# Performance work log

Hardware: AMD Instinct MI355X
Metric: run time of the kernel (lower is better)

Reference implementation:

```python
import jax, jax.numpy as jnp
from jax import lax
import numpy as np

V, E, H = 32000, 128, 256
B, S = 256, 256
A, SA = 8, 32


def gru_last(tokens, lengths, emb, Wih, Whh, bih, bhh):
    """PyTorch-GRU over padded [B,S] tokens; returns hidden at step lengths-1 ([B,H])."""
    Bb, Ss = tokens.shape
    Hh = Whh.shape[1]
    x = emb[tokens]                                   # [B,S,E]
    gi = jnp.einsum('bse,ge->bsg', x, Wih) + bih      # input gates precomputed [B,S,3H]
    lengths = jnp.maximum(lengths, 1)
    mask = jnp.arange(Ss)[None, :] < lengths[:, None]  # [B,S] valid-step mask

    def step(h, inp):
        gi_t, m_t = inp                               # [B,3H], [B]
        gh = h @ Whh.T + bhh                          # [B,3H]
        ir, iz, inn = jnp.split(gi_t, 3, axis=-1)
        hr, hz, hn = jnp.split(gh, 3, axis=-1)
        r = jax.nn.sigmoid(ir + hr)
        z = jax.nn.sigmoid(iz + hz)
        n = jnp.tanh(inn + r * hn)
        h_new = (1.0 - z) * n + z * h
        h = jnp.where(m_t[:, None], h_new, h)          # freeze past length (packed-seq semantics)
        return h, None

    h0 = jnp.zeros((Bb, Hh), x.dtype)
    hT, _ = lax.scan(step, h0, (gi.transpose(1, 0, 2), mask.T))
    return hT


def setup_inputs() -> dict:
    key = jax.random.key(0)
    ks = jax.random.split(key, 16)
    sc = 0.05
    inp = {
        'obs_tokens':  jax.random.randint(ks[0], (B, S), 0, V),
        'obs_len':     jax.random.randint(ks[1], (B,), 1, S + 1),
        'look_tokens': jax.random.randint(ks[2], (B, S), 0, V),
        'look_len':    jax.random.randint(ks[3], (B,), 1, S + 1),
        'inv_tokens':  jax.random.randint(ks[4], (B, S), 0, V),
        'inv_len':     jax.random.randint(ks[5], (B,), 1, S + 1),
        'act_tokens':  jax.random.randint(ks[6], (B * A, SA), 0, V),
        'act_len':     jax.random.randint(ks[7], (B * A,), 1, SA + 1),
        'emb':  jax.random.normal(ks[8], (V, E), jnp.float32) * sc,
        # stacked GRU params for [obs, look, inv, act] encoders
        'Wih':  jax.random.normal(ks[9],  (4, 3 * H, E), jnp.float32) * sc,
        'Whh':  jax.random.normal(ks[10], (4, 3 * H, H), jnp.float32) * sc,
        'bih':  jax.random.normal(ks[11], (4, 3 * H), jnp.float32) * sc,
        'bhh':  jax.random.normal(ks[12], (4, 3 * H), jnp.float32) * sc,
        'hidden_W': jax.random.normal(ks[13], (H, 4 * H), jnp.float32) * sc,
        'hidden_b': jnp.zeros((H,), jnp.float32),
        'scorer_W': jax.random.normal(ks[14], (1, H), jnp.float32) * sc,
        'scorer_b': jnp.zeros((1,), jnp.float32),
    }
    return inp


def reference(obs_tokens, obs_len, look_tokens, look_len, inv_tokens, inv_len,
              act_tokens, act_len, emb, Wih, Whh, bih, bhh,
              hidden_W, hidden_b, scorer_W, scorer_b):
    obs_out  = gru_last(obs_tokens,  obs_len,  emb, Wih[0], Whh[0], bih[0], bhh[0])
    look_out = gru_last(look_tokens, look_len, emb, Wih[1], Whh[1], bih[1], bhh[1])
    inv_out  = gru_last(inv_tokens,  inv_len,  emb, Wih[2], Whh[2], bih[2], bhh[2])
    act_out  = gru_last(act_tokens,  act_len,  emb, Wih[3], Whh[3], bih[3], bhh[3])

    state = jnp.concatenate([obs_out, look_out, inv_out], axis=1)  # [B,3H]
    n_act = act_tokens.shape[0] // obs_tokens.shape[0]
    state_rep = jnp.repeat(state, n_act, axis=0)                    # [B*A,3H]
    z = jax.nn.relu(jnp.concatenate([state_rep, act_out], axis=1) @ hidden_W.T + hidden_b)
    q = (z @ scorer_W.T + scorer_b)[:, 0]                           # [B*A]
    return q.reshape(obs_tokens.shape[0], n_act)                    # per-state q-values [B,A]
```

## Files before the change

### kernel.cpp

```cpp
#include <hip/hip_runtime.h>
#include <math.h>

#define VSZ 32000
#define EDIM 128
#define HDIM 256
#define BSZ 256
#define SLEN 256
#define ANUM 8
#define SALEN 32
#define G3 768
#define TB 16
#define PADW 392

#define WB_SHORTS (4 * 12 * 8 * 6 * 2 * 512)
#define KK_STRIDE (8 * 6 * 2 * 512)
#define WV_STRIDE (6 * 2 * 512)
#define OFF_HWT   (WB_SHORTS / 2)
#define HWT_SIZE  (1024 * HDIM)
#define OFF_STATE (OFF_HWT + HWT_SIZE)
#define OFF_ACT   (OFF_STATE + BSZ * G3)

typedef __attribute__((ext_vector_type(8))) short bf16x8;
typedef __attribute__((ext_vector_type(4))) short bf16x4;
typedef __attribute__((ext_vector_type(4))) float f32x4;

__device__ __forceinline__ unsigned short bf16_rne(float f) {
    unsigned int u = __builtin_bit_cast(unsigned int, f);
    unsigned int r = (u + 0x7FFFu + ((u >> 16) & 1u)) >> 16;
    return (unsigned short)r;
}
__device__ __forceinline__ float bf16_to_f32(unsigned short h) {
    unsigned int u = ((unsigned int)h) << 16;
    return __builtin_bit_cast(float, u);
}

__global__ void prep_frag(const float* __restrict__ Wih, const float* __restrict__ Whh,
                          unsigned short* __restrict__ WB) {
    int idx = blockIdx.x * 256 + threadIdx.x;
    int q = idx & 7;
    int l = (idx >> 3) & 63;
    int rest = idx >> 9;
    int slot = rest % 6; rest /= 6;
    int wv = rest & 7;   rest >>= 3;
    int kk = rest % 12;
    int enc = rest / 12;
    int cc2 = slot / 3, g3 = slot % 3;
    int row = 256 * g3 + 16 * (wv + 8 * cc2) + (l & 15);
    int kloc = 8 * (l >> 4) + q;
    float v;
    if (kk < 4) v = Wih[(enc * G3 + row) * EDIM + 32 * kk + kloc];
    else        v = Whh[(enc * G3 + row) * HDIM + 32 * (kk - 4) + kloc];
    unsigned short hi = bf16_rne(v);
    unsigned short lo = bf16_rne(v - bf16_to_f32(hi));
    size_t base = ((((size_t)(enc * 12 + kk) * 8 + wv) * 6 + slot) * 2) * 512 + l * 8 + q;
    WB[base] = hi;
    WB[base + 512] = lo;
}

__global__ void prep_hwt(const float* __restrict__ hW, float* __restrict__ hWT) {
    int idx = blockIdx.x * 256 + threadIdx.x;
    if (idx >= HWT_SIZE) return;
    int k = idx >> 8;
    int j = idx & 255;
    hWT[idx] = hW[j * 1024 + k];
}

__global__ void __launch_bounds__(1024, 1)
gru_mfma(const int* __restrict__ obs_t, const int* __restrict__ obs_l,
         const int* __restrict__ look_t, const int* __restrict__ look_l,
         const int* __restrict__ inv_t, const int* __restrict__ inv_l,
         const int* __restrict__ act_t, const int* __restrict__ act_l,
         const float* __restrict__ emb, const float* __restrict__ bih,
         const float* __restrict__ bhh, const unsigned short* __restrict__ WB,
         float* __restrict__ state, float* __restrict__ act_out) {
    const int bid = blockIdx.x;
    const int x = bid & 7, rr = bid >> 3;
    int enc, tile, S;
    const int* toks;
    const int* lens;
    if (x < 6 && rr < 8) {
        enc = x >> 1; tile = (x & 1) * 8 + rr; S = SLEN;
        toks = (enc == 0) ? obs_t : (enc == 1) ? look_t : inv_t;
        lens = (enc == 0) ? obs_l : (enc == 1) ? look_l : inv_l;
    } else {
        enc = 3; S = SALEN;
        tile = (x >= 6) ? (rr * 2 + (x - 6)) : (44 + (rr - 8) * 6 + x);
        toks = act_t; lens = act_l;
    }
    const int tid = threadIdx.x;
    const int l   = tid & 63;
    const int w   = tid >> 6;
    const int wvb = w & 7;
    const int c2  = w >> 3;
    const int lr  = l & 15;
    const int lg  = l >> 4;
    const int j   = 16 * wvb + 128 * c2 + lr;

    __shared__ __align__(16) unsigned short xh_hi[TB][PADW];
    __shared__ __align__(16) unsigned short xh_lo[TB][PADW];

    if (tid < 512) {
        int m = tid >> 5, c = tid & 31;
#pragma unroll
        for (int q = 0; q < 8; ++q) {
            xh_hi[m][EDIM + 8 * c + q] = 0;
            xh_lo[m][EDIM + 8 * c + q] = 0;
        }
    }

    int maxlen = 1;
    for (int s = 0; s < TB; ++s) {
        int L = lens[tile * TB + s];
        if (L < 1) L = 1;
        if (L > maxlen) maxlen = L;
    }
    int lenm[4];
#pragma unroll
    for (int i = 0; i < 4; ++i) {
        int L = lens[tile * TB + 4 * lg + i];
        lenm[i] = (L < 1) ? 1 : L;
    }

    const float bR  = bih[enc * G3 + j] + bhh[enc * G3 + j];
    const float bZ  = bih[enc * G3 + 256 + j] + bhh[enc * G3 + 256 + j];
    const float bIN = bih[enc * G3 + 512 + j];
    const float bHN = bhh[enc * G3 + 512 + j];

    float hO[4];
#pragma unroll
    for (int i = 0; i < 4; ++i) hO[i] = 0.f;

    auto stage = [&](int tt) {
        if (tid < 512) {
            int m = tid >> 5, g = tid & 31;
            int tok = toks[(tile * TB + m) * S + tt];
            const float4 v = *(const float4*)(emb + (size_t)tok * EDIM + g * 4);
            float vv[4] = {v.x, v.y, v.z, v.w};
            bf16x4 H, Lo;
#pragma unroll
            for (int q = 0; q < 4; ++q) {
                unsigned short h16 = bf16_rne(vv[q]);
                H[q]  = (short)h16;
                Lo[q] = (short)bf16_rne(vv[q] - bf16_to_f32(h16));
            }
            *(bf16x4*)(&xh_hi[m][g * 4]) = H;
            *(bf16x4*)(&xh_lo[m][g * 4]) = Lo;
        }
    };

    const unsigned short* WBw = WB + (size_t)enc * (12 * KK_STRIDE)
                                   + wvb * WV_STRIDE + (c2 * 3) * 1024 + l * 8;

    stage(0);
    __syncthreads();

    for (int t = 0; t < maxlen; ++t) {
        f32x4 aR  = (f32x4){bR, bR, bR, bR};
        f32x4 aZ  = (f32x4){bZ, bZ, bZ, bZ};
        f32x4 aNX = (f32x4){bIN, bIN, bIN, bIN};
        f32x4 aNH = (f32x4){bHN, bHN, bHN, bHN};

#pragma unroll 2
        for (int kk = 0; kk < 12; ++kk) {
            const int off = (kk < 4) ? 32 * kk : EDIM + 32 * (kk - 4);
            bf16x8 Ahi = *(const bf16x8*)(&xh_hi[lr][off + 8 * lg]);
            bf16x8 Alo = *(const bf16x8*)(&xh_lo[lr][off + 8 * lg]);
            const unsigned short* wb = WBw + (size_t)kk * KK_STRIDE;
            bf16x8 BhR = *(const bf16x8*)(wb);
            bf16x8 BhZ = *(const bf16x8*)(wb + 1024);
            bf16x8 BhN = *(const bf16x8*)(wb + 2048);
            aR = __builtin_amdgcn_mfma_f32_16x16x32_bf16(Ahi, BhR, aR, 0, 0, 0);
            aR = __builtin_amdgcn_mfma_f32_16x16x32_bf16(Alo, BhR, aR, 0, 0, 0);
            aZ = __builtin_amdgcn_mfma_f32_16x16x32_bf16(Ahi, BhZ, aZ, 0, 0, 0);
            aZ = __builtin_amdgcn_mfma_f32_16x16x32_bf16(Alo, BhZ, aZ, 0, 0, 0);
            if (kk < 4) {
                aNX = __builtin_amdgcn_mfma_f32_16x16x32_bf16(Ahi, BhN, aNX, 0, 0, 0);
                aNX = __builtin_amdgcn_mfma_f32_16x16x32_bf16(Alo, BhN, aNX, 0, 0, 0);
            } else {
                aNH = __builtin_amdgcn_mfma_f32_16x16x32_bf16(Ahi, BhN, aNH, 0, 0, 0);
                aNH = __builtin_amdgcn_mfma_f32_16x16x32_bf16(Alo, BhN, aNH, 0, 0, 0);
            }
        }

        __syncthreads();

#pragma unroll
        for (int i = 0; i < 4; ++i) {
            int m = 4 * lg + i;
            float r = 1.f / (1.f + expf(-aR[i]));
            float z = 1.f / (1.f + expf(-aZ[i]));
            float n = tanhf(aNX[i] + r * aNH[i]);
            float hv = (1.f - z) * n + z * hO[i];
            hv = (t < lenm[i]) ? hv : hO[i];
            hO[i] = hv;
            unsigned short h16 = bf16_rne(hv);
            xh_hi[m][EDIM + j] = h16;
            xh_lo[m][EDIM + j] = bf16_rne(hv - bf16_to_f32(h16));
        }
        if (t + 1 < maxlen) stage(t + 1);
        __syncthreads();
    }

#pragma unroll
    for (int i = 0; i < 4; ++i) {
        int sg = tile * TB + 4 * lg + i;
        if (enc < 3) state[sg * G3 + enc * HDIM + j] = hO[i];
        else         act_out[sg * HDIM + j] = hO[i];
    }
}

__global__ void __launch_bounds__(256)
mlp_kernel(const float* __restrict__ state, const float* __restrict__ act_out,
           const float* __restrict__ hWT, const float* __restrict__ hb,
           const float* __restrict__ sW, const float* __restrict__ sb,
           float* __restrict__ q) {
    int b = blockIdx.x;
    int j = threadIdx.x;
    __shared__ float st[G3];
    __shared__ float ab[ANUM][HDIM];
#pragma unroll
    for (int i = 0; i < 3; ++i) st[i * 256 + j] = state[b * G3 + i * 256 + j];
#pragma unroll
    for (int i = 0; i < ANUM; ++i) ab[i][j] = act_out[(b * ANUM + i) * HDIM + j];
    __syncthreads();

    float accS = 0.f;
#pragma unroll 4
    for (int k = 0; k < G3; ++k) accS += st[k] * hWT[k * HDIM + j];

    float accA[ANUM];
#pragma unroll
    for (int i = 0; i < ANUM; ++i) accA[i] = 0.f;
    for (int k = 0; k < HDIM; ++k) {
        float w = hWT[(G3 + k) * HDIM + j];
#pragma unroll
        for (int i = 0; i < ANUM; ++i) accA[i] += ab[i][k] * w;
    }

    float base = hb[j] + accS;
    float p[ANUM];
#pragma unroll
    for (int i = 0; i < ANUM; ++i) {
        float zz = base + accA[i];
        zz = zz > 0.f ? zz : 0.f;
        p[i] = zz * sW[j];
    }

    __shared__ float wsum[ANUM][4];
#pragma unroll
    for (int i = 0; i < ANUM; ++i) {
        float v = p[i];
        for (int off = 32; off >= 1; off >>= 1) v += __shfl_down(v, off, 64);
        if ((j & 63) == 0) wsum[i][j >> 6] = v;
    }
    __syncthreads();
    if (j < ANUM) q[b * ANUM + j] = wsum[j][0] + wsum[j][1] + wsum[j][2] + wsum[j][3] + sb[0];
}

extern "C" void kernel_launch(void* const* d_in, const int* in_sizes, int n_in,
                              void* d_out, int out_size, void* d_ws, size_t ws_size,
                              hipStream_t stream) {
    const int* obs_t  = (const int*)d_in[0];
    const int* obs_l  = (const int*)d_in[1];
    const int* look_t = (const int*)d_in[2];
    const int* look_l = (const int*)d_in[3];
    const int* inv_t  = (const int*)d_in[4];
    const int* inv_l  = (const int*)d_in[5];
    const int* act_t  = (const int*)d_in[6];
    const int* act_l  = (const int*)d_in[7];
    const float* emb  = (const float*)d_in[8];
    const float* Wih  = (const float*)d_in[9];
    const float* Whh  = (const float*)d_in[10];
    const float* bih  = (const float*)d_in[11];
    const float* bhh  = (const float*)d_in[12];
    const float* hW   = (const float*)d_in[13];
    const float* hb   = (const float*)d_in[14];
    const float* sW   = (const float*)d_in[15];
    const float* sb   = (const float*)d_in[16];

    float* ws    = (float*)d_ws;
    unsigned short* WB = (unsigned short*)d_ws;
    float* hWT   = ws + OFF_HWT;
    float* state = ws + OFF_STATE;
    float* act_o = ws + OFF_ACT;

    prep_frag<<<(WB_SHORTS / 2 + 255) / 256, 256, 0, stream>>>(Wih, Whh, WB);
    prep_hwt<<<(HWT_SIZE + 255) / 256, 256, 0, stream>>>(hW, hWT);
    gru_mfma<<<176, 1024, 0, stream>>>(obs_t, obs_l, look_t, look_l, inv_t, inv_l,
                                       act_t, act_l, emb, bih, bhh, WB,
                                       state, act_o);
    mlp_kernel<<<256, 256, 0, stream>>>(state, act_o, hWT, hb, sW, sb, (float*)d_out);
}
```

Measured before the change: 1.636 ms.

## Cache GRU weight fragments in registers and LDS across timesteps

Five of the twelve K-chunks of the gate weights (the four input chunks and the first hidden chunk) are now loaded once into registers before the time loop. Two more chunks are staged once into shared memory, and only the remaining five are re-read from global memory each step. The goal is less repeated global/L2 weight traffic on the serial recurrence. The cost is higher register pressure at 1024 threads per block and about 96KB of extra LDS, which could cause spills or exceed shared-memory limits.

New measurement: 2.637 ms. 1.61x slower.

```diff
diff --git a/kernel.cpp b/kernel.cpp
--- a/kernel.cpp
+++ b/kernel.cpp
@@ -65,6 +65,19 @@
     hWT[idx] = hW[j * 1024 + k];
 }
 
+#define MFMA_B(Ahi, Alo, BR, BZ, BN, ACCN)                                        \
+    aR   = __builtin_amdgcn_mfma_f32_16x16x32_bf16(Ahi, BR, aR, 0, 0, 0);         \
+    aR   = __builtin_amdgcn_mfma_f32_16x16x32_bf16(Alo, BR, aR, 0, 0, 0);         \
+    aZ   = __builtin_amdgcn_mfma_f32_16x16x32_bf16(Ahi, BZ, aZ, 0, 0, 0);         \
+    aZ   = __builtin_amdgcn_mfma_f32_16x16x32_bf16(Alo, BZ, aZ, 0, 0, 0);         \
+    ACCN = __builtin_amdgcn_mfma_f32_16x16x32_bf16(Ahi, BN, ACCN, 0, 0, 0);       \
+    ACCN = __builtin_amdgcn_mfma_f32_16x16x32_bf16(Alo, BN, ACCN, 0, 0, 0);
+
+#define REGKK(OFF, BR, BZ, BN, ACCN) {                                            \
+    bf16x8 Ahi_ = *(const bf16x8*)(&xh_hi[lr][(OFF) + 8 * lg]);                   \
+    bf16x8 Alo_ = *(const bf16x8*)(&xh_lo[lr][(OFF) + 8 * lg]);                   \
+    MFMA_B(Ahi_, Alo_, BR, BZ, BN, ACCN) }
+
 __global__ void __launch_bounds__(1024, 1)
 gru_mfma(const int* __restrict__ obs_t, const int* __restrict__ obs_l,
          const int* __restrict__ look_t, const int* __restrict__ look_l,
@@ -98,6 +111,7 @@
 
     __shared__ __align__(16) unsigned short xh_hi[TB][PADW];
     __shared__ __align__(16) unsigned short xh_lo[TB][PADW];
+    __shared__ __align__(16) unsigned short wlds[2][16][3][512];
 
     if (tid < 512) {
         int m = tid >> 5, c = tid & 31;
@@ -151,6 +165,29 @@
     const unsigned short* WBw = WB + (size_t)enc * (12 * KK_STRIDE)
                                    + wvb * WV_STRIDE + (c2 * 3) * 1024 + l * 8;
 
+    bf16x8 W0R = *(const bf16x8*)(WBw + (size_t)0 * KK_STRIDE);
+    bf16x8 W0Z = *(const bf16x8*)(WBw + (size_t)0 * KK_STRIDE + 1024);
+    bf16x8 W0N = *(const bf16x8*)(WBw + (size_t)0 * KK_STRIDE + 2048);
+    bf16x8 W1R = *(const bf16x8*)(WBw + (size_t)1 * KK_STRIDE);
+    bf16x8 W1Z = *(const bf16x8*)(WBw + (size_t)1 * KK_STRIDE + 1024);
+    bf16x8 W1N = *(const bf16x8*)(WBw + (size_t)1 * KK_STRIDE + 2048);
+    bf16x8 W2R = *(const bf16x8*)(WBw + (size_t)2 * KK_STRIDE);
+    bf16x8 W2Z = *(const bf16x8*)(WBw + (size_t)2 * KK_STRIDE + 1024);
+    bf16x8 W2N = *(const bf16x8*)(WBw + (size_t)2 * KK_STRIDE + 2048);
+    bf16x8 W3R = *(const bf16x8*)(WBw + (size_t)3 * KK_STRIDE);
+    bf16x8 W3Z = *(const bf16x8*)(WBw + (size_t)3 * KK_STRIDE + 1024);
+    bf16x8 W3N = *(const bf16x8*)(WBw + (size_t)3 * KK_STRIDE + 2048);
+    bf16x8 W4R = *(const bf16x8*)(WBw + (size_t)4 * KK_STRIDE);
+    bf16x8 W4Z = *(const bf16x8*)(WBw + (size_t)4 * KK_STRIDE + 1024);
+    bf16x8 W4N = *(const bf16x8*)(WBw + (size_t)4 * KK_STRIDE + 2048);
+
+#pragma unroll
+    for (int kki = 0; kki < 2; ++kki)
+#pragma unroll
+        for (int g = 0; g < 3; ++g)
+            *(bf16x8*)(&wlds[kki][w][g][l * 8]) =
+                *(const bf16x8*)(WBw + (size_t)(5 + kki) * KK_STRIDE + g * 1024);
+
     stage(0);
     __syncthreads();
 
@@ -161,26 +198,33 @@
         f32x4 aNH = (f32x4){bHN, bHN, bHN, bHN};
 
 #pragma unroll 2
-        for (int kk = 0; kk < 12; ++kk) {
-            const int off = (kk < 4) ? 32 * kk : EDIM + 32 * (kk - 4);
+        for (int kk = 7; kk < 12; ++kk) {
+            const int off = EDIM + 32 * (kk - 4);
             bf16x8 Ahi = *(const bf16x8*)(&xh_hi[lr][off + 8 * lg]);
             bf16x8 Alo = *(const bf16x8*)(&xh_lo[lr][off + 8 * lg]);
             const unsigned short* wb = WBw + (size_t)kk * KK_STRIDE;
             bf16x8 BhR = *(const bf16x8*)(wb);
             bf16x8 BhZ = *(const bf16x8*)(wb + 1024);
             bf16x8 BhN = *(const bf16x8*)(wb + 2048);
-            aR = __builtin_amdgcn_mfma_f32_16x16x32_bf16(Ahi, BhR, aR, 0, 0, 0);
-            aR = __builtin_amdgcn_mfma_f32_16x16x32_bf16(Alo, BhR, aR, 0, 0, 0);
-            aZ = __builtin_amdgcn_mfma_f32_16x16x32_bf16(Ahi, BhZ, aZ, 0, 0, 0);
-            aZ = __builtin_amdgcn_mfma_f32_16x16x32_bf16(Alo, BhZ, aZ, 0, 0, 0);
-            if (kk < 4) {
-                aNX = __builtin_amdgcn_mfma_f32_16x16x32_bf16(Ahi, BhN, aNX, 0, 0, 0);
-                aNX = __builtin_amdgcn_mfma_f32_16x16x32_bf16(Alo, BhN, aNX, 0, 0, 0);
-            } else {
-                aNH = __builtin_amdgcn_mfma_f32_16x16x32_bf16(Ahi, BhN, aNH, 0, 0, 0);
-                aNH = __builtin_amdgcn_mfma_f32_16x16x32_bf16(Alo, BhN, aNH, 0, 0, 0);
-            }
-        }
+            MFMA_B(Ahi, Alo, BhR, BhZ, BhN, aNH)
+        }
+
+#pragma unroll
+        for (int kki = 0; kki < 2; ++kki) {
+            const int off = EDIM + 32 * (1 + kki);
+            bf16x8 Ahi = *(const bf16x8*)(&xh_hi[lr][off + 8 * lg]);
+            bf16x8 Alo = *(const bf16x8*)(&xh_lo[lr][off + 8 * lg]);
+            bf16x8 BhR = *(const bf16x8*)(&wlds[kki][w][0][l * 8]);
+            bf16x8 BhZ = *(const bf16x8*)(&wlds[kki][w][1][l * 8]);
+            bf16x8 BhN = *(const bf16x8*)(&wlds[kki][w][2][l * 8]);
+            MFMA_B(Ahi, Alo, BhR, BhZ, BhN, aNH)
+        }
+
+        REGKK(0,    W0R, W0Z, W0N, aNX)
+        REGKK(32,   W1R, W1Z, W1N, aNX)
+        REGKK(64,   W2R, W2Z, W2N, aNX)
+        REGKK(96,   W3R, W3Z, W3N, aNX)
+        REGKK(EDIM, W4R, W4Z, W4N, aNH)
 
         __syncthreads();
 
```
